# Kernel optimization log

Hardware: AMD Instinct MI355X
Metric: run time of the kernel (lower is better)

## Reference

```python
import jax, jax.numpy as jnp
import numpy as np

G = 4        # split_group
H = 64       # hidden_size_t = 256 // 4 (causal -> //1)
I = 64       # input_size_t  = 256 // 4
EPS = 1e-5


def _lstm(x, W_ih, W_hh, b):
    """Grouped unidirectional LSTM, PyTorch gate order (i,f,g,o).
    x: (G,B,T,I); W_ih: (G,4H,I); W_hh: (G,4H,H); b: (G,4H) -> (G,B,T,H)"""
    g, bsz, t, _ = x.shape
    h_dim = W_hh.shape[-1]
    # precompute input projections for all timesteps
    xp = jnp.einsum('gbti,gki->gbtk', x, W_ih) + b[:, None, None, :]  # (G,B,T,4H)
    xp = jnp.moveaxis(xp, 2, 0)  # (T,G,B,4H)

    def step(carry, xt):
        h, c = carry
        gates = xt + jnp.einsum('gbh,gkh->gbk', h, W_hh)
        i_g, f_g, g_g, o_g = jnp.split(gates, 4, axis=-1)
        i_g = jax.nn.sigmoid(i_g)
        f_g = jax.nn.sigmoid(f_g)
        g_g = jnp.tanh(g_g)
        o_g = jax.nn.sigmoid(o_g)
        c = f_g * c + i_g * g_g
        h = o_g * jnp.tanh(c)
        return (h, c), h

    h0 = jnp.zeros((g, bsz, h_dim), x.dtype)
    _, hs = jax.lax.scan(step, (h0, h0), xp)  # hs: (T,G,B,H)
    return jnp.moveaxis(hs, 0, 2)  # (G,B,T,H)


def _bn(x, gamma, beta):
    """BatchNorm1d (training stats) over (B,T) per feature. x: (B,T,F)"""
    mean = x.mean(axis=(0, 1))
    var = x.var(axis=(0, 1))
    return (x - mean) * jax.lax.rsqrt(var + EPS) * gamma + beta


def setup_inputs() -> dict:
    key = jax.random.key(0)
    ks = jax.random.split(key, 12)
    s = 0.1
    F = G * H
    return {
        'inpt': jax.random.normal(ks[0], (32, 1000, 256), jnp.float32),
        'W_ih1': jax.random.normal(ks[1], (G, 4 * H, I), jnp.float32) * s,
        'W_hh1': jax.random.normal(ks[2], (G, 4 * H, H), jnp.float32) * s,
        'b1': jax.random.normal(ks[3], (G, 4 * H), jnp.float32) * s,
        'W_ih2': jax.random.normal(ks[4], (G, 4 * H, H), jnp.float32) * s,
        'W_hh2': jax.random.normal(ks[5], (G, 4 * H, H), jnp.float32) * s,
        'b2': jax.random.normal(ks[6], (G, 4 * H), jnp.float32) * s,
        'gamma1': jnp.ones((F,), jnp.float32) + jax.random.normal(ks[7], (F,)) * 0.01,
        'beta1': jax.random.normal(ks[8], (F,), jnp.float32) * 0.01,
        'gamma2': jnp.ones((F,), jnp.float32) + jax.random.normal(ks[9], (F,)) * 0.01,
        'beta2': jax.random.normal(ks[10], (F,), jnp.float32) * 0.01,
    }


def reference(inpt, W_ih1, W_hh1, b1, W_ih2, W_hh2, b2, gamma1, beta1, gamma2, beta2):
    B, T, F = inpt.shape
    # chunk along features -> (G,B,T,I)
    xg = jnp.transpose(inpt.reshape(B, T, G, I), (2, 0, 1, 3))
    y1 = _lstm(xg, W_ih1, W_hh1, b1)  # (G,B,T,H)
    # torch.stack(dim=-1) + flatten: feature index = h*G + g (interleaved)
    x = jnp.transpose(y1, (1, 2, 3, 0)).reshape(B, T, H * G)
    x = _bn(x, gamma1, beta1)
    # chunk again into G contiguous groups of size H
    xg2 = jnp.transpose(x.reshape(B, T, G, H), (2, 0, 1, 3))
    y2 = _lstm(xg2, W_ih2, W_hh2, b2)  # (G,B,T,H)
    # torch.cat(dim=-1): contiguous groups
    x = jnp.transpose(y2, (1, 2, 0, 3)).reshape(B, T, G * H)
    x = _bn(x, gamma2, beta2)
    return x
```

## Files before the change

kernel.cpp:

```cpp
#include <hip/hip_runtime.h>
#include <math.h>

#define G 4
#define H 64
#define T 1000
#define B 32
#define ROWS (B*T)

__device__ __forceinline__ float sigm(float x) {
    return 1.f / (1.f + __expf(-x));
}
__device__ __forceinline__ float tanh_f(float x) {
    return 2.f / (1.f + __expf(-2.f * x)) - 1.f;
}

__device__ __forceinline__ void wg_barrier() {
    asm volatile("s_waitcnt lgkmcnt(0)" ::: "memory");
    __builtin_amdgcn_s_barrier();
    __builtin_amdgcn_sched_barrier(0);
}

template<bool BN>
__device__ __forceinline__ void proj_body(int id,
             const float* __restrict__ xin,
             const float* __restrict__ Wih,
             const float* __restrict__ bias,
             const float* __restrict__ ac,
             float* __restrict__ xp,
             int t0, int tcn, int tcmax, int TT)
{
    const int tt = id % TT; id /= TT;
    const int b = id & 31;
    const int g = id >> 5;

    __shared__ __align__(16) float xs[64][68];
    __shared__ __align__(16) float wsm[64][68];

    const int tx = threadIdx.x & 15, ty = threadIdx.x >> 4;

    #pragma unroll
    for (int j = 0; j < 4; ++j) {
        int idx = j * 1024 + threadIdx.x * 4;
        int r = idx >> 6, ci = idx & 63;
        int tg = t0 + tt * 64 + r; if (tg > T - 1) tg = T - 1;
        float4 v = *(const float4*)&xin[((size_t)b * T + tg) * 256 + g * 64 + ci];
        if (BN) {
            float4 a4 = *(const float4*)&ac[g * 64 + ci];
            float4 c4 = *(const float4*)&ac[256 + g * 64 + ci];
            v.x = fmaf(v.x, a4.x, c4.x);
            v.y = fmaf(v.y, a4.y, c4.y);
            v.z = fmaf(v.z, a4.z, c4.z);
            v.w = fmaf(v.w, a4.w, c4.w);
        }
        *(float4*)&xs[r][ci] = v;
    }

    float* xpb = xp + (size_t)(g * 32 + b) * tcmax * 256;

    for (int kt = 0; kt < 4; ++kt) {
        __syncthreads();
        #pragma unroll
        for (int j = 0; j < 4; ++j) {
            int idx = j * 1024 + threadIdx.x * 4;
            int r = idx >> 6, ci = idx & 63;
            float4 v = *(const float4*)&Wih[(size_t)((g * 256 + kt * 64 + r) << 6) + ci];
            *(float4*)&wsm[r][ci] = v;
        }
        __syncthreads();

        float acc[4][4] = {};
        #pragma unroll
        for (int i4 = 0; i4 < 16; ++i4) {
            float4 xv[4], wv[4];
            #pragma unroll
            for (int q = 0; q < 4; ++q) xv[q] = *(const float4*)&xs[ty * 4 + q][i4 * 4];
            #pragma unroll
            for (int q = 0; q < 4; ++q) wv[q] = *(const float4*)&wsm[tx * 4 + q][i4 * 4];
            #pragma unroll
            for (int a = 0; a < 4; ++a)
                #pragma unroll
                for (int c = 0; c < 4; ++c) {
                    acc[a][c] = fmaf(xv[a].x, wv[c].x, acc[a][c]);
                    acc[a][c] = fmaf(xv[a].y, wv[c].y, acc[a][c]);
                    acc[a][c] = fmaf(xv[a].z, wv[c].z, acc[a][c]);
                    acc[a][c] = fmaf(xv[a].w, wv[c].w, acc[a][c]);
                }
        }

        const int kbase = kt * 64 + tx * 4;
        const float4 b4 = *(const float4*)&bias[g * 256 + kbase];
        #pragma unroll
        for (int a = 0; a < 4; ++a) {
            int tloc = tt * 64 + ty * 4 + a;
            if (tloc < tcn) {
                float4 o;
                o.x = acc[a][0] + b4.x;
                o.y = acc[a][1] + b4.y;
                o.z = acc[a][2] + b4.z;
                o.w = acc[a][3] + b4.w;
                *(float4*)&xpb[(size_t)tloc * 256 + kbase] = o;
            }
        }
    }
}

template<bool BN>
__global__ __launch_bounds__(256)
void xp_proj(const float* __restrict__ xin, const float* __restrict__ Wih,
             const float* __restrict__ bias, const float* __restrict__ ac,
             float* __restrict__ xp, int t0, int tcn, int tcmax, int TT)
{
    proj_body<BN>(blockIdx.x, xin, Wih, bias, ac, xp, t0, tcn, tcmax, TT);
}

template<int LAYER>
__device__ __forceinline__ void rec_body(
            const float* __restrict__ xp,
            const float* __restrict__ Whh,
            float* __restrict__ out,
            float* __restrict__ stateh, float* __restrict__ statec,
            float* __restrict__ sums,
            int t0, int t1, int tcmax)
{
    __builtin_amdgcn_s_setprio(1);
    const int blk = blockIdx.x;
    const int g = blk >> 5, b = blk & 31;
    const int l = threadIdx.x & 63, w = threadIdx.x >> 6;
    const int c16 = l & 15, gt = l >> 4;
    const int col = w * 16 + c16;
    const int row = gt * 64 + col;

    __shared__ __align__(16) float hsh[2][64];

    float whh[64];
    {
        const float4* wp = (const float4*)&Whh[(size_t)((g * 256 + row) << 6)];
        #pragma unroll
        for (int i = 0; i < 16; ++i) {
            float4 v = wp[i];
            whh[4*i] = v.x; whh[4*i+1] = v.y; whh[4*i+2] = v.z; whh[4*i+3] = v.w;
        }
    }
    const float m  = (gt == 2) ? 2.f : 1.f;
    const float A  = (gt == 2) ? 2.f : 1.f;
    const float Bc = (gt == 2) ? -1.f : 0.f;

    float cst = 0.f;
    if (t0 == 0) {
        if (threadIdx.x < 64) hsh[0][threadIdx.x] = 0.f;
    } else {
        cst = statec[blk * 64 + col];
        if (threadIdx.x < 64) hsh[0][threadIdx.x] = stateh[blk * 64 + threadIdx.x];
    }

    const float* xpb = xp + (size_t)blk * tcmax * 256 + row;
    float p[4];
    #pragma unroll
    for (int j = 0; j < 4; ++j) {
        int tp = t0 + j; if (tp > t1 - 1) tp = t1 - 1;
        p[j] = xpb[(size_t)(tp - t0) * 256];
    }

    float hl = 0.f, st_s = 0.f, st_ss = 0.f;
    __syncthreads();

    const int nsteps = t1 - t0;
    for (int s4 = 0; s4 < nsteps; s4 += 4) {
        #pragma unroll
        for (int j = 0; j < 4; ++j) {
            const int cur = j & 1;
            float a0 = 0.f, a1 = 0.f, a2 = 0.f, a3 = 0.f;
            const float4* hv = (const float4*)hsh[cur];
            #pragma unroll
            for (int q = 0; q < 16; ++q) {
                float4 z = hv[q];
                a0 = fmaf(whh[4*q],   z.x, a0);
                a1 = fmaf(whh[4*q+1], z.y, a1);
                a2 = fmaf(whh[4*q+2], z.z, a2);
                a3 = fmaf(whh[4*q+3], z.w, a3);
            }
            float pre = ((a0 + a1) + (a2 + a3)) + p[j];
            {
                int tp = t0 + s4 + j + 4; if (tp > t1 - 1) tp = t1 - 1;
                p[j] = xpb[(size_t)(tp - t0) * 256];
            }
            float act = A / (1.f + __expf(-m * pre)) + Bc;
            float gg = __shfl_xor(act, 16);
            float fg = __shfl_xor(act, 32);
            float ig = __shfl_xor(act, 48);
            cst = fmaf(fg, cst, ig * gg);
            float h = act * tanh_f(cst);
            if (gt == 3) {
                hsh[cur ^ 1][col] = h;
                int t = t0 + s4 + j;
                if (LAYER == 1) out[((size_t)b * T + t) * 256 + col * 4 + g] = h;
                else            out[((size_t)b * T + t) * 256 + g * 64 + col] = h;
                st_s += h;
                st_ss = fmaf(h, h, st_ss);
                hl = h;
            }
            wg_barrier();
        }
    }
    if (gt == 3) {
        stateh[blk * 64 + col] = hl;
        statec[blk * 64 + col] = cst;
        int f = (LAYER == 1) ? (col * 4 + g) : (g * 64 + col);
        atomicAdd(&sums[f], st_s);
        atomicAdd(&sums[256 + f], st_ss);
    }
}

template<int LAYER, bool PBN>
__global__ __launch_bounds__(256, 1)
void fused_step(const float* __restrict__ xpA, const float* __restrict__ Whh,
                float* __restrict__ out,
                float* __restrict__ stateh, float* __restrict__ statec,
                float* __restrict__ sums,
                int t0, int t1, int tcmax,
                const float* __restrict__ xin, const float* __restrict__ Wih,
                const float* __restrict__ bias, const float* __restrict__ acbn,
                float* __restrict__ xpB, int t0n, int tcnn, int TTn)
{
    if (blockIdx.x < 128) {
        rec_body<LAYER>(xpA, Whh, out, stateh, statec, sums, t0, t1, tcmax);
    } else {
        proj_body<PBN>(blockIdx.x - 128, xin, Wih, bias, acbn, xpB,
                       t0n, tcnn, tcmax, TTn);
    }
}

template<int LAYER>
__global__ __launch_bounds__(256, 1)
void rec_kernel(const float* __restrict__ xin,
                const float* __restrict__ Wih,
                const float* __restrict__ Whh,
                const float* __restrict__ bias,
                const float* __restrict__ bnac,
                float* __restrict__ out)
{
    const int g = blockIdx.x & 3;
    const int b = blockIdx.x >> 2;
    const int k = threadIdx.x;

    __shared__ __align__(16) float xsh[2][64];
    __shared__ __align__(16) float hsh[64];
    __shared__ __align__(16) float gsh[256];

    float wih[64], whh[64];
    {
        const float4* wi = (const float4*)(Wih + (size_t)(g * 256 + k) * 64);
        const float4* wh = (const float4*)(Whh + (size_t)(g * 256 + k) * 64);
        #pragma unroll
        for (int i = 0; i < 16; ++i) {
            float4 v = wi[i];
            wih[4*i] = v.x; wih[4*i+1] = v.y; wih[4*i+2] = v.z; wih[4*i+3] = v.w;
            float4 u = wh[i];
            whh[4*i] = u.x; whh[4*i+1] = u.y; whh[4*i+2] = u.z; whh[4*i+3] = u.w;
        }
    }
    const float bk = bias[g * 256 + k];
    const long rowbase = (long)b * T;
    const int  colbase = g * 64;

    float c = 0.f, af = 1.f, cf = 0.f;
    float xa = 0.f, xb = 0.f;

    if (k < 64) {
        if (LAYER == 2) { af = bnac[colbase + k]; cf = bnac[256 + colbase + k]; }
        hsh[k] = 0.f;
        float x0 = xin[(rowbase + 0) * 256 + colbase + k];
        xsh[0][k] = (LAYER == 2) ? fmaf(x0, af, cf) : x0;
        xa = xin[(rowbase + 1) * 256 + colbase + k];
        xb = xin[(rowbase + 2) * 256 + colbase + k];
    }
    __syncthreads();

    for (int t = 0; t < T; ++t) {
        const int cur = t & 1;
        float xn = 0.f;
        if (k < 64) {
            int tp = t + 3; if (tp > T - 1) tp = T - 1;
            xn = xin[(rowbase + tp) * 256 + colbase + k];
        }
        const float* xs = xsh[cur];
        float a0 = 0.f, a1 = 0.f, a2 = 0.f, a3 = 0.f;
        #pragma unroll
        for (int i = 0; i < 64; i += 4) {
            a0 = fmaf(wih[i],     xs[i],     a0);
            a1 = fmaf(wih[i + 1], xs[i + 1], a1);
            a2 = fmaf(wih[i + 2], xs[i + 2], a2);
            a3 = fmaf(wih[i + 3], xs[i + 3], a3);
        }
        #pragma unroll
        for (int jq = 0; jq < 64; jq += 4) {
            a0 = fmaf(whh[jq],     hsh[jq],     a0);
            a1 = fmaf(whh[jq + 1], hsh[jq + 1], a1);
            a2 = fmaf(whh[jq + 2], hsh[jq + 2], a2);
            a3 = fmaf(whh[jq + 3], hsh[jq + 3], a3);
        }
        const float acc = bk + ((a0 + a1) + (a2 + a3));
        const float act = (k >= 128 && k < 192) ? tanh_f(acc) : sigm(acc);
        gsh[k] = act;
        __syncthreads();

        if (k < 64) {
            const float ig = gsh[k];
            const float fg = gsh[64 + k];
            const float gg = gsh[128 + k];
            const float og = gsh[192 + k];
            c = fmaf(fg, c, ig * gg);
            const float h = og * tanh_f(c);
            hsh[k] = h;
            const long rrow = rowbase + t;
            if (LAYER == 1) out[rrow * 256 + k * 4 + g] = h;
            else            out[rrow * 256 + colbase + k] = h;
            xsh[cur ^ 1][k] = fmaf(xa, af, cf);
            xa = xb; xb = xn;
        }
        __syncthreads();
    }
}

__global__ void zero_ws(float* sums, int n) {
    int i = blockIdx.x * blockDim.x + threadIdx.x;
    if (i < n) sums[i] = 0.f;
}

__global__ __launch_bounds__(256) void stats_reduce(const float* __restrict__ x,
                                                    float* __restrict__ sums)
{
    float s = 0.f, ss = 0.f;
    for (int r = blockIdx.x; r < ROWS; r += gridDim.x) {
        float v = x[(long)r * 256 + threadIdx.x];
        s += v;
        ss = fmaf(v, v, ss);
    }
    atomicAdd(&sums[threadIdx.x], s);
    atomicAdd(&sums[256 + threadIdx.x], ss);
}

__global__ void stats_finalize(const float* __restrict__ sums,
                               const float* __restrict__ gamma,
                               const float* __restrict__ beta,
                               float* __restrict__ ac)
{
    int f = threadIdx.x;
    const float invN = 1.f / (float)ROWS;
    float mean = sums[f] * invN;
    float var  = fmaf(-mean, mean, sums[256 + f] * invN);
    float a = gamma[f] * rsqrtf(var + 1e-5f);
    ac[f]       = a;
    ac[256 + f] = fmaf(-mean, a, beta[f]);
}

__global__ __launch_bounds__(256) void bn_apply(float* __restrict__ x,
                                                const float* __restrict__ ac)
{
    __shared__ float a_s[256], c_s[256];
    a_s[threadIdx.x] = ac[threadIdx.x];
    c_s[threadIdx.x] = ac[256 + threadIdx.x];
    __syncthreads();
    const long n4 = (long)ROWS * 64;
    for (long i = (long)blockIdx.x * blockDim.x + threadIdx.x; i < n4;
         i += (long)gridDim.x * blockDim.x) {
        float4 v = ((float4*)x)[i];
        int f0 = (int)((i * 4) & 255);
        v.x = fmaf(v.x, a_s[f0],     c_s[f0]);
        v.y = fmaf(v.y, a_s[f0 + 1], c_s[f0 + 1]);
        v.z = fmaf(v.z, a_s[f0 + 2], c_s[f0 + 2]);
        v.w = fmaf(v.w, a_s[f0 + 3], c_s[f0 + 3]);
        ((float4*)x)[i] = v;
    }
}

extern "C" void kernel_launch(void* const* d_in, const int* in_sizes, int n_in,
                              void* d_out, int out_size, void* d_ws, size_t ws_size,
                              hipStream_t stream)
{
    const float* inpt   = (const float*)d_in[0];
    const float* Wih1   = (const float*)d_in[1];
    const float* Whh1   = (const float*)d_in[2];
    const float* b1     = (const float*)d_in[3];
    const float* Wih2   = (const float*)d_in[4];
    const float* Whh2   = (const float*)d_in[5];
    const float* b2     = (const float*)d_in[6];
    const float* gamma1 = (const float*)d_in[7];
    const float* beta1  = (const float*)d_in[8];
    const float* gamma2 = (const float*)d_in[9];
    const float* beta2  = (const float*)d_in[10];
    float* out  = (float*)d_out;

    float* sums1 = (float*)d_ws;
    float* sums2 = sums1 + 512;
    float* acbn1 = sums2 + 512;
    float* acbn2 = acbn1 + 512;
    float* sth   = acbn2 + 512;
    float* stc   = sth + 8192;
    float* xpb   = stc + 8192;

    const size_t fixedB = (size_t)(4 * 512 + 2 * 8192) * 4;
    const long perT = 128L * 256L * 4L;
    long availPair = ((long)ws_size - (long)fixedB) / (2L * perT);
    int Tc = (availPair >= T) ? T : (int)(availPair & ~3L);

    if (Tc >= 8) {
        float* buf[2] = { xpb, xpb + (size_t)Tc * 128 * 256 };
        const int nch = (T + Tc - 1) / Tc;
        zero_ws<<<4, 256, 0, stream>>>(sums1, 1024);

        {
            int tcn0 = (Tc < T) ? Tc : T;
            int TT0 = (tcn0 + 63) / 64;
            xp_proj<false><<<128 * TT0, 256, 0, stream>>>(
                inpt, Wih1, b1, nullptr, buf[0], 0, tcn0, Tc, TT0);
            for (int c = 0; c < nch; ++c) {
                int t0 = c * Tc;
                int t1 = t0 + Tc; if (t1 > T) t1 = T;
                int t0n = t1;
                int tcnn = (c + 1 < nch) ? ((T - t0n < Tc) ? (T - t0n) : Tc) : 0;
                int TTn = (tcnn + 63) / 64;
                fused_step<1, false><<<128 + 128 * TTn, 256, 0, stream>>>(
                    buf[c & 1], Whh1, out, sth, stc, sums1, t0, t1, Tc,
                    inpt, Wih1, b1, nullptr, buf[(c + 1) & 1], t0n, tcnn, TTn);
            }
        }
        stats_finalize<<<1, 256, 0, stream>>>(sums1, gamma1, beta1, acbn1);

        {
            int tcn0 = (Tc < T) ? Tc : T;
            int TT0 = (tcn0 + 63) / 64;
            xp_proj<true><<<128 * TT0, 256, 0, stream>>>(
                out, Wih2, b2, acbn1, buf[0], 0, tcn0, Tc, TT0);
            for (int c = 0; c < nch; ++c) {
                int t0 = c * Tc;
                int t1 = t0 + Tc; if (t1 > T) t1 = T;
                int t0n = t1;
                int tcnn = (c + 1 < nch) ? ((T - t0n < Tc) ? (T - t0n) : Tc) : 0;
                int TTn = (tcnn + 63) / 64;
                fused_step<2, true><<<128 + 128 * TTn, 256, 0, stream>>>(
                    buf[c & 1], Whh2, out, sth, stc, sums2, t0, t1, Tc,
                    out, Wih2, b2, acbn1, buf[(c + 1) & 1], t0n, tcnn, TTn);
            }
        }
        stats_finalize<<<1, 256, 0, stream>>>(sums2, gamma2, beta2, acbn2);
        bn_apply<<<2048, 256, 0, stream>>>(out, acbn2);
    } else {
        zero_ws<<<2, 256, 0, stream>>>(sums1, 512);
        rec_kernel<1><<<G * B, 256, 0, stream>>>(inpt, Wih1, Whh1, b1, nullptr, out);
        stats_reduce<<<256, 256, 0, stream>>>(out, sums1);
        stats_finalize<<<1, 256, 0, stream>>>(sums1, gamma1, beta1, acbn1);
        rec_kernel<2><<<G * B, 256, 0, stream>>>(out, Wih2, Whh2, b2, acbn1, out);
        zero_ws<<<2, 256, 0, stream>>>(sums2, 512);
        stats_reduce<<<256, 256, 0, stream>>>(out, sums2);
        stats_finalize<<<1, 256, 0, stream>>>(sums2, gamma2, beta2, acbn2);
        bn_apply<<<2048, 256, 0, stream>>>(out, acbn2);
    }
}
```

Baseline: 1.583 ms.

## Run each LSTM sequence in a single wave with fp16 dot2 recurrence

The recurrent part now runs one (group, batch) sequence per 64-lane wave, eight sequences per 512-thread block. Each lane computes all four gates for its hidden unit using fp16-packed W_hh and h with fdot2, so the per-step workgroup barrier and the cross-lane shuffles are gone. The time chunk is capped at 256 to pipeline projection with recurrence, and projection tiles are packed two per 512-thread block. This trades more registers and fewer blocks for the recurrence, plus fp16 rounding of h and W_hh that may hurt accuracy, for a lower per-step latency.

```diff
diff --git a/kernel.cpp b/kernel.cpp
--- a/kernel.cpp
+++ b/kernel.cpp
@@ -7,6 +7,24 @@
 #define B 32
 #define ROWS (B*T)
 
+typedef _Float16 f16;
+typedef _Float16 f16x2 __attribute__((ext_vector_type(2)));
+typedef _Float16 f16x8 __attribute__((ext_vector_type(8)));
+
+#if defined(__has_builtin)
+#if __has_builtin(__builtin_amdgcn_fdot2)
+#define HAVE_FDOT2 1
+#endif
+#endif
+
+__device__ __forceinline__ float dot2(f16x2 a, f16x2 b, float c) {
+#ifdef HAVE_FDOT2
+    return __builtin_amdgcn_fdot2(a, b, c, false);
+#else
+    return fmaf((float)a[0], (float)b[0], fmaf((float)a[1], (float)b[1], c));
+#endif
+}
+
 __device__ __forceinline__ float sigm(float x) {
     return 1.f / (1.f + __expf(-x));
 }
@@ -14,28 +32,235 @@
     return 2.f / (1.f + __expf(-2.f * x)) - 1.f;
 }
 
-__device__ __forceinline__ void wg_barrier() {
-    asm volatile("s_waitcnt lgkmcnt(0)" ::: "memory");
-    __builtin_amdgcn_s_barrier();
-    __builtin_amdgcn_sched_barrier(0);
+template<int LAYER>
+__device__ void rec_wave(const float* __restrict__ xp,
+                         const float* __restrict__ Whh,
+                         float* __restrict__ out,
+                         float* __restrict__ stateh, float* __restrict__ statec,
+                         float* __restrict__ sums,
+                         int t0, int t1, int tcmax)
+{
+    __builtin_amdgcn_s_setprio(1);
+    __shared__ __align__(16) _Float16 hx[8][64];
+    const int wv = threadIdx.x >> 6;
+    const int c  = threadIdx.x & 63;
+    const int sq = blockIdx.x * 8 + wv;
+    const int g = sq >> 5, b = sq & 31;
+
+    f16x2 wpk[4][32];
+    #pragma unroll
+    for (int gt = 0; gt < 4; ++gt) {
+        const float2* wp = (const float2*)&Whh[(size_t)((g * 256 + gt * 64 + c) << 6)];
+        #pragma unroll
+        for (int k = 0; k < 32; ++k) {
+            float2 v = wp[k];
+            f16x2 r; r[0] = (f16)v.x; r[1] = (f16)v.y;
+            wpk[gt][k] = r;
+        }
+    }
+
+    f16x2 hpk[32];
+    float cst;
+    if (t0 == 0) {
+        #pragma unroll
+        for (int k = 0; k < 32; ++k) { f16x2 z; z[0] = (f16)0.f; z[1] = (f16)0.f; hpk[k] = z; }
+        cst = 0.f;
+    } else {
+        const float2* sh = (const float2*)&stateh[sq * 64];
+        #pragma unroll
+        for (int k = 0; k < 32; ++k) {
+            float2 v = sh[k];
+            f16x2 r; r[0] = (f16)v.x; r[1] = (f16)v.y;
+            hpk[k] = r;
+        }
+        cst = statec[sq * 64 + c];
+    }
+
+    const float* xpb = xp + (size_t)sq * tcmax * 256;
+    float p[4][4];
+    #pragma unroll
+    for (int j = 0; j < 4; ++j) {
+        int tp = t0 + j; if (tp > t1 - 1) tp = t1 - 1;
+        #pragma unroll
+        for (int gt = 0; gt < 4; ++gt)
+            p[j][gt] = xpb[(size_t)(tp - t0) * 256 + gt * 64 + c];
+    }
+
+    float st_s = 0.f, st_ss = 0.f, hl = 0.f;
+    const int nsteps = t1 - t0;
+    for (int s4 = 0; s4 < nsteps; s4 += 4) {
+        #pragma unroll
+        for (int j = 0; j < 4; ++j) {
+            float pre[4];
+            #pragma unroll
+            for (int gt = 0; gt < 4; ++gt) {
+                float a0 = 0.f, a1 = 0.f;
+                #pragma unroll
+                for (int k = 0; k < 32; k += 2) {
+                    a0 = dot2(wpk[gt][k],     hpk[k],     a0);
+                    a1 = dot2(wpk[gt][k + 1], hpk[k + 1], a1);
+                }
+                pre[gt] = (a0 + a1) + p[j][gt];
+            }
+            {
+                int tp = t0 + s4 + j + 4; if (tp > t1 - 1) tp = t1 - 1;
+                #pragma unroll
+                for (int gt = 0; gt < 4; ++gt)
+                    p[j][gt] = xpb[(size_t)(tp - t0) * 256 + gt * 64 + c];
+            }
+            float ig = sigm(pre[0]);
+            float fg = sigm(pre[1]);
+            float gg = tanh_f(pre[2]);
+            float og = sigm(pre[3]);
+            cst = fmaf(fg, cst, ig * gg);
+            float h = og * tanh_f(cst);
+            int t = t0 + s4 + j;
+            if (LAYER == 1) out[((size_t)b * T + t) * 256 + c * 4 + g] = h;
+            else            out[((size_t)b * T + t) * 256 + g * 64 + c] = h;
+            st_s += h;
+            st_ss = fmaf(h, h, st_ss);
+            hl = h;
+            hx[wv][c] = (f16)h;
+            const f16x8* hp8 = (const f16x8*)&hx[wv][0];
+            #pragma unroll
+            for (int q = 0; q < 8; ++q) {
+                f16x8 v = hp8[q];
+                f16x2 r0; r0[0] = v[0]; r0[1] = v[1];
+                f16x2 r1; r1[0] = v[2]; r1[1] = v[3];
+                f16x2 r2; r2[0] = v[4]; r2[1] = v[5];
+                f16x2 r3; r3[0] = v[6]; r3[1] = v[7];
+                hpk[q * 4 + 0] = r0; hpk[q * 4 + 1] = r1;
+                hpk[q * 4 + 2] = r2; hpk[q * 4 + 3] = r3;
+            }
+        }
+    }
+    stateh[sq * 64 + c] = hl;
+    statec[sq * 64 + c] = cst;
+    int f = (LAYER == 1) ? (c * 4 + g) : (g * 64 + c);
+    atomicAdd(&sums[f], st_s);
+    atomicAdd(&sums[256 + f], st_ss);
 }
 
 template<bool BN>
-__device__ __forceinline__ void proj_body(int id,
-             const float* __restrict__ xin,
-             const float* __restrict__ Wih,
-             const float* __restrict__ bias,
-             const float* __restrict__ ac,
-             float* __restrict__ xp,
-             int t0, int tcn, int tcmax, int TT)
-{
+__device__ void proj_tile512(int tile, bool active,
+                             const float* __restrict__ xin,
+                             const float* __restrict__ Wih,
+                             const float* __restrict__ bias,
+                             const float* __restrict__ ac,
+                             float* __restrict__ xp,
+                             int t0, int tcn, int tcmax, int TT)
+{
+    __shared__ __align__(16) float xs[2][64][68];
+    __shared__ __align__(16) float wsm[2][64][68];
+    const int hf  = threadIdx.x >> 8;
+    const int tid = threadIdx.x & 255;
+
+    int id = tile;
     const int tt = id % TT; id /= TT;
     const int b = id & 31;
     const int g = id >> 5;
 
+    const int tx = tid & 15, ty = tid >> 4;
+
+    #pragma unroll
+    for (int j = 0; j < 4; ++j) {
+        int idx = j * 1024 + tid * 4;
+        int r = idx >> 6, ci = idx & 63;
+        int tg = t0 + tt * 64 + r; if (tg > T - 1) tg = T - 1;
+        float4 v = *(const float4*)&xin[((size_t)b * T + tg) * 256 + g * 64 + ci];
+        if (BN) {
+            float4 a4 = *(const float4*)&ac[g * 64 + ci];
+            float4 c4 = *(const float4*)&ac[256 + g * 64 + ci];
+            v.x = fmaf(v.x, a4.x, c4.x);
+            v.y = fmaf(v.y, a4.y, c4.y);
+            v.z = fmaf(v.z, a4.z, c4.z);
+            v.w = fmaf(v.w, a4.w, c4.w);
+        }
+        *(float4*)&xs[hf][r][ci] = v;
+    }
+
+    float* xpb = xp + (size_t)(g * 32 + b) * tcmax * 256;
+
+    for (int kt = 0; kt < 4; ++kt) {
+        __syncthreads();
+        #pragma unroll
+        for (int j = 0; j < 4; ++j) {
+            int idx = j * 1024 + tid * 4;
+            int r = idx >> 6, ci = idx & 63;
+            float4 v = *(const float4*)&Wih[(size_t)((g * 256 + kt * 64 + r) << 6) + ci];
+            *(float4*)&wsm[hf][r][ci] = v;
+        }
+        __syncthreads();
+
+        float acc[4][4] = {};
+        #pragma unroll
+        for (int i4 = 0; i4 < 16; ++i4) {
+            float4 xv[4], wv[4];
+            #pragma unroll
+            for (int q = 0; q < 4; ++q) xv[q] = *(const float4*)&xs[hf][ty * 4 + q][i4 * 4];
+            #pragma unroll
+            for (int q = 0; q < 4; ++q) wv[q] = *(const float4*)&wsm[hf][tx * 4 + q][i4 * 4];
+            #pragma unroll
+            for (int a = 0; a < 4; ++a)
+                #pragma unroll
+                for (int cc = 0; cc < 4; ++cc) {
+                    acc[a][cc] = fmaf(xv[a].x, wv[cc].x, acc[a][cc]);
+                    acc[a][cc] = fmaf(xv[a].y, wv[cc].y, acc[a][cc]);
+                    acc[a][cc] = fmaf(xv[a].z, wv[cc].z, acc[a][cc]);
+                    acc[a][cc] = fmaf(xv[a].w, wv[cc].w, acc[a][cc]);
+                }
+        }
+
+        const int kbase = kt * 64 + tx * 4;
+        const float4 b4 = *(const float4*)&bias[g * 256 + kbase];
+        #pragma unroll
+        for (int a = 0; a < 4; ++a) {
+            int tloc = tt * 64 + ty * 4 + a;
+            if (active && tloc < tcn) {
+                float4 o;
+                o.x = acc[a][0] + b4.x;
+                o.y = acc[a][1] + b4.y;
+                o.z = acc[a][2] + b4.z;
+                o.w = acc[a][3] + b4.w;
+                *(float4*)&xpb[(size_t)tloc * 256 + kbase] = o;
+            }
+        }
+    }
+}
+
+template<int LAYER, bool PBN>
+__global__ __launch_bounds__(512, 2)
+void fused2(const float* __restrict__ xpA, const float* __restrict__ Whh,
+            float* __restrict__ out,
+            float* __restrict__ stateh, float* __restrict__ statec,
+            float* __restrict__ sums,
+            int t0, int t1, int tcmax,
+            const float* __restrict__ xin, const float* __restrict__ Wih,
+            const float* __restrict__ bias, const float* __restrict__ acbn,
+            float* __restrict__ xpB, int t0n, int tcnn, int TTn, int ntiles)
+{
+    if (blockIdx.x < 16) {
+        rec_wave<LAYER>(xpA, Whh, out, stateh, statec, sums, t0, t1, tcmax);
+    } else {
+        int tile0 = (blockIdx.x - 16) * 2 + (threadIdx.x >> 8);
+        bool act = tile0 < ntiles;
+        int tile = act ? tile0 : (ntiles > 0 ? ntiles - 1 : 0);
+        proj_tile512<PBN>(tile, act, xin, Wih, bias, acbn, xpB, t0n, tcnn, tcmax, TTn);
+    }
+}
+
+template<bool BN>
+__global__ __launch_bounds__(256)
+void xp_proj(const float* __restrict__ xin, const float* __restrict__ Wih,
+             const float* __restrict__ bias, const float* __restrict__ ac,
+             float* __restrict__ xp, int t0, int tcn, int tcmax, int TT)
+{
     __shared__ __align__(16) float xs[64][68];
     __shared__ __align__(16) float wsm[64][68];
-
+    int id = blockIdx.x;
+    const int tt = id % TT; id /= TT;
+    const int b = id & 31;
+    const int g = id >> 5;
     const int tx = threadIdx.x & 15, ty = threadIdx.x >> 4;
 
     #pragma unroll
@@ -56,7 +281,6 @@
     }
 
     float* xpb = xp + (size_t)(g * 32 + b) * tcmax * 256;
-
     for (int kt = 0; kt < 4; ++kt) {
         __syncthreads();
         #pragma unroll
@@ -79,11 +303,11 @@
             #pragma unroll
             for (int a = 0; a < 4; ++a)
                 #pragma unroll
-                for (int c = 0; c < 4; ++c) {
-                    acc[a][c] = fmaf(xv[a].x, wv[c].x, acc[a][c]);
-                    acc[a][c] = fmaf(xv[a].y, wv[c].y, acc[a][c]);
-                    acc[a][c] = fmaf(xv[a].z, wv[c].z, acc[a][c]);
-                    acc[a][c] = fmaf(xv[a].w, wv[c].w, acc[a][c]);
+                for (int cc = 0; cc < 4; ++cc) {
+                    acc[a][cc] = fmaf(xv[a].x, wv[cc].x, acc[a][cc]);
+                    acc[a][cc] = fmaf(xv[a].y, wv[cc].y, acc[a][cc]);
+                    acc[a][cc] = fmaf(xv[a].z, wv[cc].z, acc[a][cc]);
+                    acc[a][cc] = fmaf(xv[a].w, wv[cc].w, acc[a][cc]);
                 }
         }
 
@@ -101,132 +325,6 @@
                 *(float4*)&xpb[(size_t)tloc * 256 + kbase] = o;
             }
         }
-    }
-}
-
-template<bool BN>
-__global__ __launch_bounds__(256)
-void xp_proj(const float* __restrict__ xin, const float* __restrict__ Wih,
-             const float* __restrict__ bias, const float* __restrict__ ac,
-             float* __restrict__ xp, int t0, int tcn, int tcmax, int TT)
-{
-    proj_body<BN>(blockIdx.x, xin, Wih, bias, ac, xp, t0, tcn, tcmax, TT);
-}
-
-template<int LAYER>
-__device__ __forceinline__ void rec_body(
-            const float* __restrict__ xp,
-            const float* __restrict__ Whh,
-            float* __restrict__ out,
-            float* __restrict__ stateh, float* __restrict__ statec,
-            float* __restrict__ sums,
-            int t0, int t1, int tcmax)
-{
-    __builtin_amdgcn_s_setprio(1);
-    const int blk = blockIdx.x;
-    const int g = blk >> 5, b = blk & 31;
-    const int l = threadIdx.x & 63, w = threadIdx.x >> 6;
-    const int c16 = l & 15, gt = l >> 4;
-    const int col = w * 16 + c16;
-    const int row = gt * 64 + col;
-
-    __shared__ __align__(16) float hsh[2][64];
-
-    float whh[64];
-    {
-        const float4* wp = (const float4*)&Whh[(size_t)((g * 256 + row) << 6)];
-        #pragma unroll
-        for (int i = 0; i < 16; ++i) {
-            float4 v = wp[i];
-            whh[4*i] = v.x; whh[4*i+1] = v.y; whh[4*i+2] = v.z; whh[4*i+3] = v.w;
-        }
-    }
-    const float m  = (gt == 2) ? 2.f : 1.f;
-    const float A  = (gt == 2) ? 2.f : 1.f;
-    const float Bc = (gt == 2) ? -1.f : 0.f;
-
-    float cst = 0.f;
-    if (t0 == 0) {
-        if (threadIdx.x < 64) hsh[0][threadIdx.x] = 0.f;
-    } else {
-        cst = statec[blk * 64 + col];
-        if (threadIdx.x < 64) hsh[0][threadIdx.x] = stateh[blk * 64 + threadIdx.x];
-    }
-
-    const float* xpb = xp + (size_t)blk * tcmax * 256 + row;
-    float p[4];
-    #pragma unroll
-    for (int j = 0; j < 4; ++j) {
-        int tp = t0 + j; if (tp > t1 - 1) tp = t1 - 1;
-        p[j] = xpb[(size_t)(tp - t0) * 256];
-    }
-
-    float hl = 0.f, st_s = 0.f, st_ss = 0.f;
-    __syncthreads();
-
-    const int nsteps = t1 - t0;
-    for (int s4 = 0; s4 < nsteps; s4 += 4) {
-        #pragma unroll
-        for (int j = 0; j < 4; ++j) {
-            const int cur = j & 1;
-            float a0 = 0.f, a1 = 0.f, a2 = 0.f, a3 = 0.f;
-            const float4* hv = (const float4*)hsh[cur];
-            #pragma unroll
-            for (int q = 0; q < 16; ++q) {
-                float4 z = hv[q];
-                a0 = fmaf(whh[4*q],   z.x, a0);
-                a1 = fmaf(whh[4*q+1], z.y, a1);
-                a2 = fmaf(whh[4*q+2], z.z, a2);
-                a3 = fmaf(whh[4*q+3], z.w, a3);
-            }
-            float pre = ((a0 + a1) + (a2 + a3)) + p[j];
-            {
-                int tp = t0 + s4 + j + 4; if (tp > t1 - 1) tp = t1 - 1;
-                p[j] = xpb[(size_t)(tp - t0) * 256];
-            }
-            float act = A / (1.f + __expf(-m * pre)) + Bc;
-            float gg = __shfl_xor(act, 16);
-            float fg = __shfl_xor(act, 32);
-            float ig = __shfl_xor(act, 48);
-            cst = fmaf(fg, cst, ig * gg);
-            float h = act * tanh_f(cst);
-            if (gt == 3) {
-                hsh[cur ^ 1][col] = h;
-                int t = t0 + s4 + j;
-                if (LAYER == 1) out[((size_t)b * T + t) * 256 + col * 4 + g] = h;
-                else            out[((size_t)b * T + t) * 256 + g * 64 + col] = h;
-                st_s += h;
-                st_ss = fmaf(h, h, st_ss);
-                hl = h;
-            }
-            wg_barrier();
-        }
-    }
-    if (gt == 3) {
-        stateh[blk * 64 + col] = hl;
-        statec[blk * 64 + col] = cst;
-        int f = (LAYER == 1) ? (col * 4 + g) : (g * 64 + col);
-        atomicAdd(&sums[f], st_s);
-        atomicAdd(&sums[256 + f], st_ss);
-    }
-}
-
-template<int LAYER, bool PBN>
-__global__ __launch_bounds__(256, 1)
-void fused_step(const float* __restrict__ xpA, const float* __restrict__ Whh,
-                float* __restrict__ out,
-                float* __restrict__ stateh, float* __restrict__ statec,
-                float* __restrict__ sums,
-                int t0, int t1, int tcmax,
-                const float* __restrict__ xin, const float* __restrict__ Wih,
-                const float* __restrict__ bias, const float* __restrict__ acbn,
-                float* __restrict__ xpB, int t0n, int tcnn, int TTn)
-{
-    if (blockIdx.x < 128) {
-        rec_body<LAYER>(xpA, Whh, out, stateh, statec, sums, t0, t1, tcmax);
-    } else {
-        proj_body<PBN>(blockIdx.x - 128, xin, Wih, bias, acbn, xpB,
-                       t0n, tcnn, tcmax, TTn);
     }
 }
 
@@ -402,7 +500,7 @@
     const size_t fixedB = (size_t)(4 * 512 + 2 * 8192) * 4;
     const long perT = 128L * 256L * 4L;
     long availPair = ((long)ws_size - (long)fixedB) / (2L * perT);
-    int Tc = (availPair >= T) ? T : (int)(availPair & ~3L);
+    int Tc = (availPair >= 256) ? 256 : (int)(availPair & ~3L);
 
     if (Tc >= 8) {
         float* buf[2] = { xpb, xpb + (size_t)Tc * 128 * 256 };
@@ -420,9 +518,11 @@
                 int t0n = t1;
                 int tcnn = (c + 1 < nch) ? ((T - t0n < Tc) ? (T - t0n) : Tc) : 0;
                 int TTn = (tcnn + 63) / 64;
-                fused_step<1, false><<<128 + 128 * TTn, 256, 0, stream>>>(
+                int ntiles = 128 * TTn;
+                int grid = 16 + (ntiles + 1) / 2;
+                fused2<1, false><<<grid, 512, 0, stream>>>(
                     buf[c & 1], Whh1, out, sth, stc, sums1, t0, t1, Tc,
-                    inpt, Wih1, b1, nullptr, buf[(c + 1) & 1], t0n, tcnn, TTn);
+                    inpt, Wih1, b1, nullptr, buf[(c + 1) & 1], t0n, tcnn, TTn, ntiles);
             }
         }
         stats_finalize<<<1, 256, 0, stream>>>(sums1, gamma1, beta1, acbn1);
@@ -438,9 +538,11 @@
                 int t0n = t1;
                 int tcnn = (c + 1 < nch) ? ((T - t0n < Tc) ? (T - t0n) : Tc) : 0;
                 int TTn = (tcnn + 63) / 64;
-                fused_step<2, true><<<128 + 128 * TTn, 256, 0, stream>>>(
+                int ntiles = 128 * TTn;
+                int grid = 16 + (ntiles + 1) / 2;
+                fused2<2, true><<<grid, 512, 0, stream>>>(
                     buf[c & 1], Whh2, out, sth, stc, sums2, t0, t1, Tc,
-                    out, Wih2, b2, acbn1, buf[(c + 1) & 1], t0n, tcnn, TTn);
+                    out, Wih2, b2, acbn1, buf[(c + 1) & 1], t0n, tcnn, TTn, ntiles);
             }
         }
         stats_finalize<<<1, 256, 0, stream>>>(sums2, gamma2, beta2, acbn2);
```

Result: slower. 3.754 ms (+137.2%).
